# Kernel tuning notes

Hardware: AMD Instinct MI355X
Metric: run time of the kernel (lower is better)

## Reference

```python
import jax, jax.numpy as jnp
import numpy as np

TAU = 0.1
NEG_EUCLID_DIST = 5.0
COS_EPS = 1e-8


def setup_inputs() -> dict:
    key = jax.random.key(0)
    k1, k2, k3, k4 = jax.random.split(key, 4)
    bs, N, F, S = 4, 8192, 512, 2048
    velo_feat = jax.random.normal(k1, (bs, N, F), dtype=jnp.float32)
    # points in a ~100m cube so the 5m negative-distance mask is a mix of True/False
    velo_pts = jax.random.uniform(k2, (bs, N, 3), dtype=jnp.float32) * 100.0
    ref_feat = jax.random.normal(k3, (bs, N, F), dtype=jnp.float32)
    matches = jax.random.randint(k4, (bs, S, 2), 0, N, dtype=jnp.int64)
    return {"velo_feat": velo_feat, "velo_pts": velo_pts, "ref_feat": ref_feat, "matches": matches}


def _gather(x, idx, width):
    # x: [bs, N, width], idx: [bs, S, 1] -> [bs, S, width]
    bs, S, _ = idx.shape
    return jnp.take_along_axis(x, jnp.broadcast_to(idx, (bs, S, width)), axis=1)


def reference(velo_feat, velo_pts, ref_feat, matches):
    bs, _, F = velo_feat.shape
    anchor_feat = _gather(velo_feat, matches[..., 0:1], F)   # [bs,S,F]
    anchor_pts = _gather(velo_pts, matches[..., 0:1], 3)     # [bs,S,3]
    pos_feat = _gather(ref_feat, matches[..., 1:2], F)       # [bs,S,F]

    # cosine similarity (torch: dot / clamp(|a|*|b|, eps))
    dot = jnp.sum(anchor_feat * pos_feat, axis=-1)
    norms = jnp.linalg.norm(anchor_feat, axis=-1) * jnp.linalg.norm(pos_feat, axis=-1)
    d_pos = (dot / jnp.maximum(norms, COS_EPS))[..., None]   # [bs,S,1]

    # raw (unnormalized) similarity matrix
    D = jnp.einsum('bsf,btf->bst', anchor_feat, pos_feat)    # [bs,S,S]
    D_cat = jnp.concatenate([d_pos, D], axis=2)              # [bs,S,S+1]

    # squared pairwise distance; compare against r^2 (equiv to cdist > r, avoids sqrt)
    sq = jnp.sum(anchor_pts * anchor_pts, axis=-1)           # [bs,S]
    d2 = sq[:, :, None] + sq[:, None, :] - 2.0 * jnp.einsum('bsd,btd->bst', anchor_pts, anchor_pts)
    far = d2 > NEG_EUCLID_DIST * NEG_EUCLID_DIST             # [bs,S,S] bool
    neg_mask = jnp.concatenate([jnp.ones_like(far[:, :, :1]), far], axis=-1)

    denom = jnp.sum(jnp.exp(D_cat / TAU) * neg_mask, axis=-1, keepdims=True)
    loss = -jnp.log(jnp.exp(d_pos / TAU) / denom)            # [bs,S,1]
    return loss.mean()
```

## Files before the change

### kernel.cpp

```cpp
#include <hip/hip_runtime.h>
#include <hip/hip_bf16.h>
#include <cmath>

#define BS 4
#define NP 8192
#define FD 512
#define SM 2048
#define LOG2E10 14.4269504088896340736f
#define LN2 0.6931471805599453f

typedef __attribute__((ext_vector_type(8))) short short8;
typedef __attribute__((ext_vector_type(4))) float f32x4;

static __device__ __forceinline__ unsigned short f2bf(float f) {
  unsigned u = __float_as_uint(f);
  unsigned r = u + 0x7fffu + ((u >> 16) & 1u);
  return (unsigned short)(r >> 16);
}
static __device__ __forceinline__ ushort4 f2bf4(float4 v) {
  ushort4 o;
  o.x = f2bf(v.x); o.y = f2bf(v.y); o.z = f2bf(v.z); o.w = f2bf(v.w);
  return o;
}

__global__ __launch_bounds__(256) void stats_k(
    const float* __restrict__ velo_feat, const float* __restrict__ velo_pts,
    const float* __restrict__ ref_feat, const int* __restrict__ matches,
    float4* __restrict__ pts4, float* __restrict__ dpos,
    unsigned short* __restrict__ Abf, unsigned short* __restrict__ Pbf)
{
  const int row = blockIdx.x * 4 + (threadIdx.x >> 6);
  const int lane = threadIdx.x & 63;
  const int b = row >> 11;
  const int ai = matches[2 * row + 0];
  const int pi = matches[2 * row + 1];

  const float4* ar = (const float4*)(velo_feat + ((size_t)b * NP + ai) * FD);
  const float4* pr = (const float4*)(ref_feat + ((size_t)b * NP + pi) * FD);
  float4 a0 = ar[lane], a1 = ar[lane + 64];
  float4 p0 = pr[lane], p1 = pr[lane + 64];

  *(ushort4*)(Abf + (size_t)row * FD + lane * 4) = f2bf4(a0);
  *(ushort4*)(Abf + (size_t)row * FD + 256 + lane * 4) = f2bf4(a1);
  *(ushort4*)(Pbf + (size_t)row * FD + lane * 4) = f2bf4(p0);
  *(ushort4*)(Pbf + (size_t)row * FD + 256 + lane * 4) = f2bf4(p1);

  float dot = a0.x * p0.x + a0.y * p0.y + a0.z * p0.z + a0.w * p0.w +
              a1.x * p1.x + a1.y * p1.y + a1.z * p1.z + a1.w * p1.w;
  float na = a0.x * a0.x + a0.y * a0.y + a0.z * a0.z + a0.w * a0.w +
             a1.x * a1.x + a1.y * a1.y + a1.z * a1.z + a1.w * a1.w;
  float nb = p0.x * p0.x + p0.y * p0.y + p0.z * p0.z + p0.w * p0.w +
             p1.x * p1.x + p1.y * p1.y + p1.z * p1.z + p1.w * p1.w;
#pragma unroll
  for (int off = 32; off; off >>= 1) {
    dot += __shfl_xor(dot, off);
    na += __shfl_xor(na, off);
    nb += __shfl_xor(nb, off);
  }
  if (lane == 0) {
    dpos[row] = dot / fmaxf(sqrtf(na) * sqrtf(nb), 1e-8f);
    const float* pp = velo_pts + ((size_t)b * NP + ai) * 3;
    float x = pp[0], y = pp[1], z = pp[2];
    pts4[row] = make_float4(x, y, z, x * x + y * y + z * z);
  }
}

__global__ __launch_bounds__(256) void tile_k(
    const unsigned short* __restrict__ Abf, const unsigned short* __restrict__ Pbf,
    const float4* __restrict__ pts4,
    float* __restrict__ maxs, float* __restrict__ sums)
{
  __shared__ unsigned short As[128 * 64];
  __shared__ unsigned short Bs[128 * 64];
  __shared__ float4 rp[128];
  __shared__ float4 cp[128];

  const int ctile = blockIdx.x, stile = blockIdx.y, b = blockIdx.z;
  const int s0 = stile * 128, c0 = ctile * 128;
  const int tid = threadIdx.x;
  const int wid = tid >> 6, lane = tid & 63;
  const int wr = wid >> 1, wc = wid & 1;
  const int cg = lane >> 4, cr = lane & 15;

  if (tid < 128) rp[tid] = pts4[(size_t)b * SM + s0 + tid];
  else           cp[tid - 128] = pts4[(size_t)b * SM + c0 + (tid - 128)];

  const char* Ab = (const char*)(Abf + ((size_t)b * SM + s0) * FD);
  const char* Bb = (const char*)(Pbf + ((size_t)b * SM + c0) * FD);

  int srow[4], soff[4];
#pragma unroll
  for (int i = 0; i < 4; i++) {
    const int L = (wid * 4 + i) * 1024 + lane * 16;
    srow[i] = L >> 7;
    const int c = L & 127;
    soff[i] = c ^ ((srow[i] & 7) << 4);
  }

  f32x4 acc[4][4];
#pragma unroll
  for (int m = 0; m < 4; m++)
#pragma unroll
    for (int n = 0; n < 4; n++) acc[m][n] = (f32x4){0.f, 0.f, 0.f, 0.f};

  for (int kk = 0; kk < FD * 2; kk += 128) {
    __syncthreads();
#pragma unroll
    for (int i = 0; i < 4; i++) {
      const int chunk = wid * 4 + i;
      __builtin_amdgcn_global_load_lds(
          (const __attribute__((address_space(1))) void*)(Ab + (size_t)srow[i] * (FD * 2) + kk + soff[i]),
          (__attribute__((address_space(3))) void*)((char*)As + chunk * 1024),
          16, 0, 0);
      __builtin_amdgcn_global_load_lds(
          (const __attribute__((address_space(1))) void*)(Bb + (size_t)srow[i] * (FD * 2) + kk + soff[i]),
          (__attribute__((address_space(3))) void*)((char*)Bs + chunk * 1024),
          16, 0, 0);
    }
    __syncthreads();

#pragma unroll
    for (int ks = 0; ks < 2; ks++) {
      short8 af[4], bfr[4];
#pragma unroll
      for (int m = 0; m < 4; m++) {
        const int r = wr * 64 + m * 16 + cr;
        const int x = (ks * 64 + cg * 16) ^ ((r & 7) << 4);
        af[m] = *(const short8*)((const char*)As + r * 128 + x);
      }
#pragma unroll
      for (int n = 0; n < 4; n++) {
        const int r = wc * 64 + n * 16 + cr;
        const int x = (ks * 64 + cg * 16) ^ ((r & 7) << 4);
        bfr[n] = *(const short8*)((const char*)Bs + r * 128 + x);
      }
#pragma unroll
      for (int m = 0; m < 4; m++)
#pragma unroll
        for (int n = 0; n < 4; n++)
          acc[m][n] = __builtin_amdgcn_mfma_f32_16x16x32_bf16(af[m], bfr[n],
                                                              acc[m][n], 0, 0, 0);
    }
  }

  const int ct32 = ctile * 2 + wc;
  float4 cv[4];
#pragma unroll
  for (int n = 0; n < 4; n++) cv[n] = cp[wc * 64 + n * 16 + cr];

#pragma unroll
  for (int m = 0; m < 4; m++) {
#pragma unroll
    for (int r = 0; r < 4; r++) {
      const int rit = wr * 64 + m * 16 + cg * 4 + r;
      float4 rv = rp[rit];
      float l[4];
      float vmax = -INFINITY;
#pragma unroll
      for (int n = 0; n < 4; n++) {
        float d2 = rv.w + cv[n].w -
                   2.f * (rv.x * cv[n].x + rv.y * cv[n].y + rv.z * cv[n].z);
        l[n] = (d2 > 25.f) ? acc[m][n][r] * LOG2E10 : -INFINITY;
        vmax = fmaxf(vmax, l[n]);
      }
#pragma unroll
      for (int off = 1; off < 16; off <<= 1)
        vmax = fmaxf(vmax, __shfl_xor(vmax, off, 16));
      float vs = 0.f;
#pragma unroll
      for (int n = 0; n < 4; n++)
        vs += (l[n] == -INFINITY) ? 0.f : exp2f(l[n] - vmax);
#pragma unroll
      for (int off = 1; off < 16; off <<= 1) vs += __shfl_xor(vs, off, 16);
      if (cr == 0) {
        size_t base = ((size_t)ct32 * BS + b) * SM + s0 + rit;
        maxs[base] = vmax;
        sums[base] = vs;
      }
    }
  }
}

__global__ __launch_bounds__(256) void rowloss_k(
    const float* __restrict__ dpos, const float* __restrict__ maxs,
    const float* __restrict__ sums, double* __restrict__ partial)
{
  const int r = blockIdx.x * 256 + threadIdx.x;
  float l0 = dpos[r] * LOG2E10;
  float M = l0;
#pragma unroll 8
  for (int c = 0; c < 32; c++) M = fmaxf(M, maxs[(size_t)c * BS * SM + r]);
  float s = exp2f(l0 - M);
#pragma unroll 8
  for (int c = 0; c < 32; c++) {
    float mc = maxs[(size_t)c * BS * SM + r];
    float sc = sums[(size_t)c * BS * SM + r];
    s += (mc == -INFINITY) ? 0.f : sc * exp2f(mc - M);
  }
  double v = (double)(LN2 * (M + log2f(s) - l0));
#pragma unroll
  for (int off = 32; off; off >>= 1) v += __shfl_down(v, off);
  __shared__ double red[4];
  if ((threadIdx.x & 63) == 0) red[threadIdx.x >> 6] = v;
  __syncthreads();
  if (threadIdx.x == 0)
    partial[blockIdx.x] = red[0] + red[1] + red[2] + red[3];
}

__global__ __launch_bounds__(64) void final_k(const double* __restrict__ partial,
                                              float* __restrict__ out)
{
  const int t = threadIdx.x;
  double v = (t < 32) ? partial[t] : 0.0;
#pragma unroll
  for (int off = 32; off; off >>= 1) v += __shfl_down(v, off);
  if (t == 0) out[0] = (float)(v / (double)(BS * SM));
}

extern "C" void kernel_launch(void* const* d_in, const int* in_sizes, int n_in,
                              void* d_out, int out_size, void* d_ws, size_t ws_size,
                              hipStream_t stream)
{
  const float* velo_feat = (const float*)d_in[0];
  const float* velo_pts  = (const float*)d_in[1];
  const float* ref_feat  = (const float*)d_in[2];
  const int*   matches   = (const int*)d_in[3];

  char* ws = (char*)d_ws;
  const size_t NBF = (size_t)BS * SM * FD * 2;
  unsigned short* Abf = (unsigned short*)ws;
  unsigned short* Pbf = (unsigned short*)(ws + NBF);
  float4* pts4 = (float4*)(ws + 2 * NBF);
  float*  dpos = (float*)(ws + 2 * NBF + (size_t)BS * SM * 16);
  float*  maxs = (float*)(ws + 2 * NBF + (size_t)BS * SM * 20);
  float*  sums = (float*)(ws + 2 * NBF + (size_t)BS * SM * 20 + (size_t)32 * BS * SM * 4);
  double* partial = (double*)(ws + 2 * NBF + (size_t)BS * SM * 20 + (size_t)64 * BS * SM * 4);

  stats_k<<<BS * SM / 4, 256, 0, stream>>>(velo_feat, velo_pts, ref_feat,
                                           matches, pts4, dpos, Abf, Pbf);
  tile_k<<<dim3(16, 16, BS), 256, 0, stream>>>(Abf, Pbf, pts4, maxs, sums);
  rowloss_k<<<BS * SM / 256, 256, 0, stream>>>(dpos, maxs, sums, partial);
  final_k<<<1, 64, 0, stream>>>(partial, (float*)d_out);
}
```

Measured before the change: 76.52 us.

## Double-buffer LDS tiles and transpose MFMA operands for a cheaper softmax epilogue

The GEMM tile kernel now double-buffers its A and B LDS tiles, issuing the next K-slice's global-to-LDS loads before computing on the current one, so there is one barrier per iteration instead of two. The MFMA operands are swapped so each lane holds a single row across its accumulator registers. The per-row max and sum then need only two cross-lane shuffles instead of a 16-lane reduction for every row. Point coordinates are read directly from global memory instead of being staged in LDS, and the -inf guard in rowloss is dropped because exp2 of -inf already yields zero. LDS use doubles to 64KB per block, which may cut occupancy.

After: 73.42 us. -4.1%, faster.

```diff
diff --git a/kernel.cpp b/kernel.cpp
--- a/kernel.cpp
+++ b/kernel.cpp
@@ -70,10 +70,8 @@
     const float4* __restrict__ pts4,
     float* __restrict__ maxs, float* __restrict__ sums)
 {
-  __shared__ unsigned short As[128 * 64];
-  __shared__ unsigned short Bs[128 * 64];
-  __shared__ float4 rp[128];
-  __shared__ float4 cp[128];
+  __shared__ unsigned short As[2][8192];
+  __shared__ unsigned short Bs[2][8192];
 
   const int ctile = blockIdx.x, stile = blockIdx.y, b = blockIdx.z;
   const int s0 = stile * 128, c0 = ctile * 128;
@@ -82,9 +80,6 @@
   const int wr = wid >> 1, wc = wid & 1;
   const int cg = lane >> 4, cr = lane & 15;
 
-  if (tid < 128) rp[tid] = pts4[(size_t)b * SM + s0 + tid];
-  else           cp[tid - 128] = pts4[(size_t)b * SM + c0 + (tid - 128)];
-
   const char* Ab = (const char*)(Abf + ((size_t)b * SM + s0) * FD);
   const char* Bb = (const char*)(Pbf + ((size_t)b * SM + c0) * FD);
 
@@ -93,32 +88,39 @@
   for (int i = 0; i < 4; i++) {
     const int L = (wid * 4 + i) * 1024 + lane * 16;
     srow[i] = L >> 7;
-    const int c = L & 127;
-    soff[i] = c ^ ((srow[i] & 7) << 4);
-  }
+    soff[i] = (L & 127) ^ ((srow[i] & 7) << 4);
+  }
+
+#define STAGE(buf, kk)                                                         \
+  do {                                                                         \
+    _Pragma("unroll") for (int i = 0; i < 4; i++) {                            \
+      const int chunk = wid * 4 + i;                                           \
+      __builtin_amdgcn_global_load_lds(                                        \
+          (const __attribute__((address_space(1))) void*)(                     \
+              Ab + ((size_t)srow[i] << 10) + (kk) + soff[i]),                  \
+          (__attribute__((address_space(3))) void*)(&As[buf][chunk * 512]),    \
+          16, 0, 0);                                                           \
+      __builtin_amdgcn_global_load_lds(                                        \
+          (const __attribute__((address_space(1))) void*)(                     \
+              Bb + ((size_t)srow[i] << 10) + (kk) + soff[i]),                  \
+          (__attribute__((address_space(3))) void*)(&Bs[buf][chunk * 512]),    \
+          16, 0, 0);                                                           \
+    }                                                                          \
+  } while (0)
 
   f32x4 acc[4][4];
 #pragma unroll
-  for (int m = 0; m < 4; m++)
-#pragma unroll
-    for (int n = 0; n < 4; n++) acc[m][n] = (f32x4){0.f, 0.f, 0.f, 0.f};
-
-  for (int kk = 0; kk < FD * 2; kk += 128) {
-    __syncthreads();
-#pragma unroll
-    for (int i = 0; i < 4; i++) {
-      const int chunk = wid * 4 + i;
-      __builtin_amdgcn_global_load_lds(
-          (const __attribute__((address_space(1))) void*)(Ab + (size_t)srow[i] * (FD * 2) + kk + soff[i]),
-          (__attribute__((address_space(3))) void*)((char*)As + chunk * 1024),
-          16, 0, 0);
-      __builtin_amdgcn_global_load_lds(
-          (const __attribute__((address_space(1))) void*)(Bb + (size_t)srow[i] * (FD * 2) + kk + soff[i]),
-          (__attribute__((address_space(3))) void*)((char*)Bs + chunk * 1024),
-          16, 0, 0);
-    }
-    __syncthreads();
-
+  for (int n = 0; n < 4; n++)
+#pragma unroll
+    for (int m = 0; m < 4; m++) acc[n][m] = (f32x4){0.f, 0.f, 0.f, 0.f};
+
+  STAGE(0, 0);
+  __syncthreads();
+
+  for (int t = 0; t < 8; ++t) {
+    if (t < 7) STAGE((t + 1) & 1, (t + 1) * 128);
+    const unsigned short* Asb = As[t & 1];
+    const unsigned short* Bsb = Bs[t & 1];
 #pragma unroll
     for (int ks = 0; ks < 2; ks++) {
       short8 af[4], bfr[4];
@@ -126,59 +128,76 @@
       for (int m = 0; m < 4; m++) {
         const int r = wr * 64 + m * 16 + cr;
         const int x = (ks * 64 + cg * 16) ^ ((r & 7) << 4);
-        af[m] = *(const short8*)((const char*)As + r * 128 + x);
+        af[m] = *(const short8*)((const char*)Asb + r * 128 + x);
       }
 #pragma unroll
       for (int n = 0; n < 4; n++) {
         const int r = wc * 64 + n * 16 + cr;
         const int x = (ks * 64 + cg * 16) ^ ((r & 7) << 4);
-        bfr[n] = *(const short8*)((const char*)Bs + r * 128 + x);
+        bfr[n] = *(const short8*)((const char*)Bsb + r * 128 + x);
       }
 #pragma unroll
-      for (int m = 0; m < 4; m++)
-#pragma unroll
-        for (int n = 0; n < 4; n++)
-          acc[m][n] = __builtin_amdgcn_mfma_f32_16x16x32_bf16(af[m], bfr[n],
-                                                              acc[m][n], 0, 0, 0);
+      for (int n = 0; n < 4; n++)
+#pragma unroll
+        for (int m = 0; m < 4; m++)
+          acc[n][m] = __builtin_amdgcn_mfma_f32_16x16x32_bf16(bfr[n], af[m],
+                                                              acc[n][m], 0, 0, 0);
     }
-  }
-
-  const int ct32 = ctile * 2 + wc;
-  float4 cv[4];
-#pragma unroll
-  for (int n = 0; n < 4; n++) cv[n] = cp[wc * 64 + n * 16 + cr];
-
-#pragma unroll
-  for (int m = 0; m < 4; m++) {
-#pragma unroll
-    for (int r = 0; r < 4; r++) {
-      const int rit = wr * 64 + m * 16 + cg * 4 + r;
-      float4 rv = rp[rit];
-      float l[4];
-      float vmax = -INFINITY;
-#pragma unroll
-      for (int n = 0; n < 4; n++) {
-        float d2 = rv.w + cv[n].w -
-                   2.f * (rv.x * cv[n].x + rv.y * cv[n].y + rv.z * cv[n].z);
-        l[n] = (d2 > 25.f) ? acc[m][n][r] * LOG2E10 : -INFINITY;
-        vmax = fmaxf(vmax, l[n]);
-      }
-#pragma unroll
-      for (int off = 1; off < 16; off <<= 1)
-        vmax = fmaxf(vmax, __shfl_xor(vmax, off, 16));
-      float vs = 0.f;
-#pragma unroll
-      for (int n = 0; n < 4; n++)
-        vs += (l[n] == -INFINITY) ? 0.f : exp2f(l[n] - vmax);
-#pragma unroll
-      for (int off = 1; off < 16; off <<= 1) vs += __shfl_xor(vs, off, 16);
-      if (cr == 0) {
-        size_t base = ((size_t)ct32 * BS + b) * SM + s0 + rit;
-        maxs[base] = vmax;
-        sums[base] = vs;
+    if (t < 7) __syncthreads();
+  }
+
+  const float4* rpg = pts4 + (size_t)b * SM + s0 + wr * 64;
+  const float4* cpg = pts4 + (size_t)b * SM + c0 + wc * 64;
+  float4 rv[4];
+#pragma unroll
+  for (int m = 0; m < 4; m++) rv[m] = rpg[m * 16 + cr];
+
+  float mx[4] = {-INFINITY, -INFINITY, -INFINITY, -INFINITY};
+#pragma unroll
+  for (int n = 0; n < 4; n++) {
+#pragma unroll
+    for (int reg = 0; reg < 4; reg++) {
+      float4 cv = cpg[n * 16 + cg * 4 + reg];
+#pragma unroll
+      for (int m = 0; m < 4; m++) {
+        float dot = rv[m].x * cv.x + rv[m].y * cv.y + rv[m].z * cv.z;
+        float d2 = rv[m].w + cv.w - 2.f * dot;
+        float l = (d2 > 25.f) ? acc[n][m][reg] * LOG2E10 : -INFINITY;
+        acc[n][m][reg] = l;
+        mx[m] = fmaxf(mx[m], l);
       }
     }
   }
+  float mxc[4], sm[4];
+#pragma unroll
+  for (int m = 0; m < 4; m++) {
+    mx[m] = fmaxf(mx[m], __shfl_xor(mx[m], 16));
+    mx[m] = fmaxf(mx[m], __shfl_xor(mx[m], 32));
+    mxc[m] = fmaxf(mx[m], -1e37f);
+    sm[m] = 0.f;
+  }
+#pragma unroll
+  for (int n = 0; n < 4; n++)
+#pragma unroll
+    for (int reg = 0; reg < 4; reg++)
+#pragma unroll
+      for (int m = 0; m < 4; m++)
+        sm[m] += exp2f(acc[n][m][reg] - mxc[m]);
+#pragma unroll
+  for (int m = 0; m < 4; m++) {
+    sm[m] += __shfl_xor(sm[m], 16);
+    sm[m] += __shfl_xor(sm[m], 32);
+  }
+  if (cg == 0) {
+    const int ct32 = ctile * 2 + wc;
+    size_t base = ((size_t)ct32 * BS + b) * SM + s0 + wr * 64;
+#pragma unroll
+    for (int m = 0; m < 4; m++) {
+      maxs[base + m * 16 + cr] = mx[m];
+      sums[base + m * 16 + cr] = sm[m];
+    }
+  }
+#undef STAGE
 }
 
 __global__ __launch_bounds__(256) void rowloss_k(
@@ -195,7 +214,7 @@
   for (int c = 0; c < 32; c++) {
     float mc = maxs[(size_t)c * BS * SM + r];
     float sc = sums[(size_t)c * BS * SM + r];
-    s += (mc == -INFINITY) ? 0.f : sc * exp2f(mc - M);
+    s += sc * exp2f(mc - M);
   }
   double v = (double)(LN2 * (M + log2f(s) - l0));
 #pragma unroll
```
